# Kernel optimization log

Measured on AMD Instinct MI355X. Metric: run time of the kernel, lower is better.

Reference implementation:

```python
import jax, jax.numpy as jnp
import numpy as np

K = 5
NUM_CLASSES = 100


def setup_inputs() -> dict:
    key = jax.random.key(0)
    k1, k2, k3 = jax.random.split(key, 3)
    x = jax.random.normal(k1, (2048, 512), dtype=jnp.float32)
    x_train = jax.random.normal(k2, (65536, 512), dtype=jnp.float32)
    y_train = jax.random.randint(k3, (65536,), 0, NUM_CLASSES, dtype=jnp.int64)
    return {"x": x, "x_train": x_train, "y_train": y_train}


def reference(x, x_train, y_train):
    # Euclidean cdist via the expansion ||a-b||^2 = ||a||^2 + ||b||^2 - 2 a.b
    x2 = jnp.sum(x * x, axis=-1, keepdims=True)            # [B, 1]
    t2 = jnp.sum(x_train * x_train, axis=-1)               # [N]
    d2 = x2 + t2[None, :] - 2.0 * (x @ x_train.T)          # [B, N]
    dists = jnp.sqrt(jnp.maximum(d2, 0.0))
    # k smallest distances -> top_k of negated distances
    _, idx = jax.lax.top_k(-dists, K)                      # idx: [B, K]
    labels = y_train[idx]                                  # [B, K]
    # mode over the K neighbor labels via per-class vote counts;
    # argmax returns the smallest label among ties (matches torch.mode tie-break)
    counts = jnp.sum(jax.nn.one_hot(labels, NUM_CLASSES, dtype=jnp.int32), axis=1)  # [B, C]
    preds = jnp.argmax(counts, axis=-1)
    return preds
```

## Files before the change

kernel.cpp:

```cpp
#include <hip/hip_runtime.h>

#define NTRAIN 65536
#define NQ     2048
#define KD     512
#define KNN    5

#define QT2 256
#define TPB 2048
#define CH 256
#define NGRP (NTRAIN / TPB)
#define NQT2 (NQ / QT2)
#define NSLOT (NGRP * KNN)
#define MARGIN 2.0f
#define CAP 128

typedef short short8 __attribute__((ext_vector_type(8)));
typedef float f32x4 __attribute__((ext_vector_type(4)));

__device__ inline unsigned short f2bf(float f) {
    unsigned u = __float_as_uint(f);
    unsigned r = u + 0x7fffu + ((u >> 16) & 1u);
    return (unsigned short)(r >> 16);
}

template<int KK>
__device__ inline void ins5(float (&bd)[KK], int (&bi)[KK], float nd, int ni) {
    if (nd < bd[KK-1] || (nd == bd[KK-1] && ni < bi[KK-1])) {
#pragma unroll
        for (int k = 0; k < KK; ++k) {
            bool sw = (nd < bd[k]) || (nd == bd[k] && ni < bi[k]);
            float od = bd[k]; int oi = bi[k];
            bd[k] = sw ? nd : od; bi[k] = sw ? ni : oi;
            nd = sw ? od : nd;    ni = sw ? oi : ni;
        }
    }
}

__device__ inline void ins5v(float (&b5)[KNN], float v) {
    if (v < b5[KNN-1]) {
#pragma unroll
        for (int k = 0; k < KNN; ++k) {
            bool sw = v < b5[k];
            float o = b5[k];
            b5[k] = sw ? v : o;
            v = sw ? o : v;
        }
    }
}

__global__ __launch_bounds__(256)
void t2_kernel(const float* __restrict__ xt, float* __restrict__ t2) {
    int row  = blockIdx.x * 4 + (threadIdx.x >> 6);
    int lane = threadIdx.x & 63;
    const float4* p = (const float4*)(xt + (size_t)row * KD);
    float s = 0.f;
#pragma unroll
    for (int c = 0; c < 2; ++c) {
        float4 v = p[lane + c * 64];
        s += v.x * v.x + v.y * v.y + v.z * v.z + v.w * v.w;
    }
#pragma unroll
    for (int off = 32; off; off >>= 1) s += __shfl_down(s, off);
    if (lane == 0) t2[row] = s;
}

__global__ __launch_bounds__(256)
void conv_perm_kernel(const float* __restrict__ in, unsigned short* __restrict__ outp) {
    __shared__ unsigned short tile[16][512];
    const int rg = blockIdx.x, t = threadIdx.x;
    const int row_l = t >> 4, sub = t & 15;

    const float* rp = in + ((size_t)rg * 16 + row_l) * KD + sub * 4;
#pragma unroll
    for (int j = 0; j < 8; ++j) {
        float4 v = *(const float4*)(rp + j * 64);
        unsigned short us[4] = { f2bf(v.x), f2bf(v.y), f2bf(v.z), f2bf(v.w) };
        *(unsigned long long*)&tile[row_l][sub * 4 + j * 64] = *(const unsigned long long*)us;
    }
    __syncthreads();

    const int kt = t >> 4;
    unsigned short* ub = outp + (size_t)(((rg >> 4) * 16 + kt) * 16 + (rg & 15)) * 512;
#pragma unroll
    for (int i = 0; i < 4; ++i) {
        int l = sub * 4 + i;
        *(uint4*)(ub + l * 8) = *(const uint4*)&tile[l & 15][kt * 32 + ((l >> 4) << 3)];
    }
}

__global__ __launch_bounds__(1024)
void knn_filter(const unsigned short* __restrict__ xperm, const unsigned short* __restrict__ xtperm,
                const float* __restrict__ t2g,
                float* __restrict__ candD, int* __restrict__ candI) {
    __shared__ __align__(16) char smem[81920];

    const int tid  = threadIdx.x;
    const int w    = tid >> 6, lane = tid & 63;
    const int wm   = w & 3,  wn = w >> 2;
    const int lrow = lane & 15, lhi = lane >> 4;

    const int qt   = blockIdx.x >> 5;
    const int grp  = blockIdx.x & 31;
    const int q0   = qt * QT2;
    const int row0 = grp * TPB;

    const char* Au = (const char*)xtperm + (size_t)grp * (8 * 16 * 16 * 1024);
    const char* Bu = (const char*)xperm  + (size_t)qt  * (16 * 16 * 1024);
    const int laneOff = lane * 16;

    f32x4 acc[4][4];
#pragma unroll
    for (int m = 0; m < 4; ++m)
#pragma unroll
        for (int n = 0; n < 4; ++n) acc[m][n] = 0.f;

    float bd[4][KNN]; int bi[4][KNN];
#pragma unroll
    for (int n = 0; n < 4; ++n)
#pragma unroll
        for (int k = 0; k < KNN; ++k) { bd[n][k] = 3.4e38f; bi[n][k] = 0x7fffffff; }

    for (int ch = 0; ch < 8; ++ch) {
#pragma unroll 2
        for (int kt = 0; kt < 16; ++kt) {
            const char* Ak = Au + (size_t)(((ch * 16 + kt) * 16) + wm * 4) * 1024 + laneOff;
            const char* Bk = Bu + (size_t)((kt * 16) + wn * 4) * 1024 + laneOff;
            short8 a0 = *(const short8*)(Ak);
            short8 a1 = *(const short8*)(Ak + 1024);
            short8 a2 = *(const short8*)(Ak + 2048);
            short8 a3 = *(const short8*)(Ak + 3072);
            short8 b0 = *(const short8*)(Bk);
            short8 b1 = *(const short8*)(Bk + 1024);
            short8 b2 = *(const short8*)(Bk + 2048);
            short8 b3 = *(const short8*)(Bk + 3072);
            acc[0][0] = __builtin_amdgcn_mfma_f32_16x16x32_bf16(a0, b0, acc[0][0], 0, 0, 0);
            acc[0][1] = __builtin_amdgcn_mfma_f32_16x16x32_bf16(a0, b1, acc[0][1], 0, 0, 0);
            acc[0][2] = __builtin_amdgcn_mfma_f32_16x16x32_bf16(a0, b2, acc[0][2], 0, 0, 0);
            acc[0][3] = __builtin_amdgcn_mfma_f32_16x16x32_bf16(a0, b3, acc[0][3], 0, 0, 0);
            acc[1][0] = __builtin_amdgcn_mfma_f32_16x16x32_bf16(a1, b0, acc[1][0], 0, 0, 0);
            acc[1][1] = __builtin_amdgcn_mfma_f32_16x16x32_bf16(a1, b1, acc[1][1], 0, 0, 0);
            acc[1][2] = __builtin_amdgcn_mfma_f32_16x16x32_bf16(a1, b2, acc[1][2], 0, 0, 0);
            acc[1][3] = __builtin_amdgcn_mfma_f32_16x16x32_bf16(a1, b3, acc[1][3], 0, 0, 0);
            acc[2][0] = __builtin_amdgcn_mfma_f32_16x16x32_bf16(a2, b0, acc[2][0], 0, 0, 0);
            acc[2][1] = __builtin_amdgcn_mfma_f32_16x16x32_bf16(a2, b1, acc[2][1], 0, 0, 0);
            acc[2][2] = __builtin_amdgcn_mfma_f32_16x16x32_bf16(a2, b2, acc[2][2], 0, 0, 0);
            acc[2][3] = __builtin_amdgcn_mfma_f32_16x16x32_bf16(a2, b3, acc[2][3], 0, 0, 0);
            acc[3][0] = __builtin_amdgcn_mfma_f32_16x16x32_bf16(a3, b0, acc[3][0], 0, 0, 0);
            acc[3][1] = __builtin_amdgcn_mfma_f32_16x16x32_bf16(a3, b1, acc[3][1], 0, 0, 0);
            acc[3][2] = __builtin_amdgcn_mfma_f32_16x16x32_bf16(a3, b2, acc[3][2], 0, 0, 0);
            acc[3][3] = __builtin_amdgcn_mfma_f32_16x16x32_bf16(a3, b3, acc[3][3], 0, 0, 0);
        }

        {
            const int c0  = row0 + ch * CH;
            const int rbl = wm * 64 + lhi * 4;
#pragma unroll
            for (int m = 0; m < 4; ++m) {
                const float4 t2v = *(const float4*)(t2g + c0 + rbl + m * 16);
#pragma unroll
                for (int n = 0; n < 4; ++n)
#pragma unroll
                    for (int r2 = 0; r2 < 4; ++r2) {
                        float sc = fmaf(-2.f, acc[m][n][r2], (&t2v.x)[r2]);
                        ins5(bd[n], bi[n], sc, c0 + rbl + m * 16 + r2);
                    }
            }
#pragma unroll
            for (int m = 0; m < 4; ++m)
#pragma unroll
                for (int n = 0; n < 4; ++n) acc[m][n] = 0.f;
        }
    }

    float* MD = (float*)smem;
    int*   MI = (int*)(smem + 40960);
    const int slot = wm * 4 + lhi;
#pragma unroll
    for (int half = 0; half < 2; ++half) {
        __syncthreads();
#pragma unroll
        for (int n = 0; n < 4; ++n) {
            const int ql = wn * 64 + n * 16 + lrow;
            if ((ql >> 7) == half) {
#pragma unroll
                for (int k = 0; k < KNN; ++k) {
                    MD[(ql & 127) * 80 + slot * KNN + k] = bd[n][k];
                    MI[(ql & 127) * 80 + slot * KNN + k] = bi[n][k];
                }
            }
        }
        __syncthreads();
        if (tid < 128) {
            float fd[KNN]; int fi[KNN];
#pragma unroll
            for (int k = 0; k < KNN; ++k) { fd[k] = 3.4e38f; fi[k] = 0x7fffffff; }
            for (int j = 0; j < 16 * KNN; ++j) ins5(fd, fi, MD[tid * 80 + j], MI[tid * 80 + j]);
            size_t base = ((size_t)(q0 + half * 128 + tid) * NGRP + grp) * KNN;
#pragma unroll
            for (int k = 0; k < KNN; ++k) { candD[base + k] = fd[k]; candI[base + k] = fi[k]; }
        }
    }
}

__global__ __launch_bounds__(256)
void knn_refine(const float* __restrict__ x, const float* __restrict__ xt,
                const float* __restrict__ t2,
                const float* __restrict__ candD, const int* __restrict__ candI,
                const int* __restrict__ y, int* __restrict__ out) {
    __shared__ float sv[256 * KNN];
    __shared__ float sv2[64 * KNN];
    __shared__ float xl[KD];
    __shared__ int   lidx[CAP];
    __shared__ float lex[CAP];
    __shared__ int   lcount;
    __shared__ float sT;

    const int q = blockIdx.x, tid = threadIdx.x;
    const float* cd = candD + (size_t)q * NSLOT;
    const int*   ci = candI + (size_t)q * NSLOT;

    for (int i = tid; i < KD; i += 256) xl[i] = x[(size_t)q * KD + i];

    float b5[KNN];
#pragma unroll
    for (int k = 0; k < KNN; ++k) b5[k] = 3.4e38f;
    for (int j = tid; j < NSLOT; j += 256) ins5v(b5, cd[j]);
#pragma unroll
    for (int k = 0; k < KNN; ++k) sv[tid * KNN + k] = b5[k];
    __syncthreads();

    if (tid < 64) {
#pragma unroll
        for (int k = 0; k < KNN; ++k) b5[k] = 3.4e38f;
        for (int t = 0; t < 4; ++t)
#pragma unroll
            for (int k = 0; k < KNN; ++k) ins5v(b5, sv[(tid * 4 + t) * KNN + k]);
#pragma unroll
        for (int k = 0; k < KNN; ++k) sv2[tid * KNN + k] = b5[k];
    }
    __syncthreads();

    if (tid == 0) {
#pragma unroll
        for (int k = 0; k < KNN; ++k) b5[k] = 3.4e38f;
        for (int j = 0; j < 64 * KNN; ++j) ins5v(b5, sv2[j]);
        sT = b5[KNN - 1] + MARGIN;
        lcount = 0;
    }
    __syncthreads();
    float T = sT;

    for (int j = tid; j < NSLOT; j += 256) {
        if (cd[j] <= T) {
            int p = atomicAdd(&lcount, 1);
            if (p < CAP) lidx[p] = ci[j];
        }
    }
    __syncthreads();
    int Q = min(lcount, CAP);

    for (int j = tid; j < Q; j += 256) {
        int c = lidx[j];
        const float* tr = xt + (size_t)c * KD;
        float s = 0.f;
        for (int k = 0; k < KD; ++k) s = fmaf(xl[k], tr[k], s);
        lex[j] = fmaf(-2.f, s, t2[c]);
    }
    __syncthreads();

    if (tid == 0) {
        bool is64 = true;
#pragma unroll
        for (int i = 1; i < 64; i += 2) is64 = is64 && (y[i] == 0);
        float fd[KNN]; int fi[KNN];
#pragma unroll
        for (int k = 0; k < KNN; ++k) { fd[k] = 3.4e38f; fi[k] = 0x7fffffff; }
        for (int j = 0; j < Q; ++j) ins5(fd, fi, lex[j], lidx[j]);
        int lab[KNN];
#pragma unroll
        for (int k = 0; k < KNN; ++k) lab[k] = is64 ? y[2 * fi[k]] : y[fi[k]];
        int bestLab = 0x7fffffff, bestC = 0;
#pragma unroll
        for (int i = 0; i < KNN; ++i) {
            int c = 0;
#pragma unroll
            for (int j = 0; j < KNN; ++j) c += (lab[j] == lab[i]);
            if (c > bestC || (c == bestC && lab[i] < bestLab)) { bestC = c; bestLab = lab[i]; }
        }
        out[q] = bestLab;
    }
}

#define FB_QT 64
#define FB_TT 64
#define FB_KT 32
#define FB_NCHUNK 32
#define FB_CHUNK (NTRAIN / FB_NCHUNK)

__global__ __launch_bounds__(256)
void fb_knn_partial(const float* __restrict__ x, const float* __restrict__ xt,
                    const float* __restrict__ t2,
                    float* __restrict__ candD, int* __restrict__ candI) {
    __shared__ __align__(16) float smem[FB_QT * 81 * 2];
    float (*Xs)[FB_QT + 4] = (float (*)[FB_QT + 4])smem;
    float (*Ts)[FB_TT + 4] = (float (*)[FB_TT + 4])(smem + FB_KT * (FB_QT + 4));
    float (*MD)[81]     = (float (*)[81])smem;
    int   (*MI)[81]     = (int   (*)[81])(smem + FB_QT * 81);

    const int tid = threadIdx.x;
    const int tx = tid & 15, ty = tid >> 4;
    const int q0 = blockIdx.x * FB_QT;
    const int c0 = blockIdx.y * FB_CHUNK;
    const int sq = tid >> 2, sc = tid & 3;

    float bd[4][KNN]; int bi_[4][KNN];
#pragma unroll
    for (int i = 0; i < 4; ++i)
#pragma unroll
        for (int k = 0; k < KNN; ++k) { bd[i][k] = 3.4e38f; bi_[i][k] = 0x7fffffff; }

    const float* xrow = x + (size_t)(q0 + sq) * KD;

    for (int s = 0; s < FB_CHUNK; s += FB_TT) {
        float acc[4][4];
#pragma unroll
        for (int i = 0; i < 4; ++i)
#pragma unroll
            for (int j = 0; j < 4; ++j) acc[i][j] = 0.f;
        const float* trow = xt + (size_t)(c0 + s + sq) * KD;
        for (int kt = 0; kt < KD; kt += FB_KT) {
            float4 xv0 = *(const float4*)(xrow + kt + sc * 8);
            float4 xv1 = *(const float4*)(xrow + kt + sc * 8 + 4);
            float4 tv0 = *(const float4*)(trow + kt + sc * 8);
            float4 tv1 = *(const float4*)(trow + kt + sc * 8 + 4);
            __syncthreads();
            Xs[sc*8+0][sq] = xv0.x; Xs[sc*8+1][sq] = xv0.y;
            Xs[sc*8+2][sq] = xv0.z; Xs[sc*8+3][sq] = xv0.w;
            Xs[sc*8+4][sq] = xv1.x; Xs[sc*8+5][sq] = xv1.y;
            Xs[sc*8+6][sq] = xv1.z; Xs[sc*8+7][sq] = xv1.w;
            Ts[sc*8+0][sq] = tv0.x; Ts[sc*8+1][sq] = tv0.y;
            Ts[sc*8+2][sq] = tv0.z; Ts[sc*8+3][sq] = tv0.w;
            Ts[sc*8+4][sq] = tv1.x; Ts[sc*8+5][sq] = tv1.y;
            Ts[sc*8+6][sq] = tv1.z; Ts[sc*8+7][sq] = tv1.w;
            __syncthreads();
#pragma unroll
            for (int k = 0; k < FB_KT; ++k) {
                const float4 av = *(const float4*)&Xs[k][ty * 4];
                const float4 bv = *(const float4*)&Ts[k][tx * 4];
                float a[4] = {av.x, av.y, av.z, av.w};
                float b[4] = {bv.x, bv.y, bv.z, bv.w};
#pragma unroll
                for (int i = 0; i < 4; ++i)
#pragma unroll
                    for (int j = 0; j < 4; ++j)
                        acc[i][j] = fmaf(a[i], b[j], acc[i][j]);
            }
        }
#pragma unroll
        for (int j = 0; j < 4; ++j) {
            int tcol = c0 + s + tx * 4 + j;
            float tt = t2[tcol];
#pragma unroll
            for (int i = 0; i < 4; ++i)
                ins5(bd[i], bi_[i], fmaf(-2.0f, acc[i][j], tt), tcol);
        }
    }
    __syncthreads();
#pragma unroll
    for (int i = 0; i < 4; ++i)
#pragma unroll
        for (int k = 0; k < KNN; ++k) {
            MD[ty * 4 + i][tx * KNN + k] = bd[i][k];
            MI[ty * 4 + i][tx * KNN + k] = bi_[i][k];
        }
    __syncthreads();
    if (tid < FB_QT) {
        int q = q0 + tid;
        for (int k = 0; k < KNN; ++k) {
            float best = 3.4e38f; int bidx = 0x7fffffff; int bj = -1;
            for (int j = 0; j < 16 * KNN; ++j) {
                float dv = MD[tid][j]; int iv = MI[tid][j];
                if (dv < best || (dv == best && iv < bidx)) { best = dv; bidx = iv; bj = j; }
            }
            MD[tid][bj] = 3.4e38f;
            candD[((size_t)q * FB_NCHUNK + blockIdx.y) * KNN + k] = best;
            candI[((size_t)q * FB_NCHUNK + blockIdx.y) * KNN + k] = bidx;
        }
    }
}

__global__ __launch_bounds__(256)
void fb_knn_final(const float* __restrict__ candD, const int* __restrict__ candI,
                  const int* __restrict__ y, int* __restrict__ out) {
    int q = blockIdx.x * 256 + threadIdx.x;
    if (q >= NQ) return;
    bool is64 = true;
#pragma unroll
    for (int i = 1; i < 64; i += 2) is64 = is64 && (y[i] == 0);
    float bd[KNN]; int bi_[KNN];
#pragma unroll
    for (int k = 0; k < KNN; ++k) { bd[k] = 3.4e38f; bi_[k] = 0x7fffffff; }
    for (int c = 0; c < FB_NCHUNK * KNN; ++c)
        ins5(bd, bi_, candD[(size_t)q * FB_NCHUNK * KNN + c], candI[(size_t)q * FB_NCHUNK * KNN + c]);
    int lab[KNN];
#pragma unroll
    for (int k = 0; k < KNN; ++k) lab[k] = is64 ? y[2 * bi_[k]] : y[bi_[k]];
    int bestLab = 0x7fffffff, bestC = 0;
#pragma unroll
    for (int i = 0; i < KNN; ++i) {
        int c = 0;
#pragma unroll
        for (int j = 0; j < KNN; ++j) c += (lab[j] == lab[i]);
        if (c > bestC || (c == bestC && lab[i] < bestLab)) { bestC = c; bestLab = lab[i]; }
    }
    out[q] = bestLab;
}

extern "C" void kernel_launch(void* const* d_in, const int* in_sizes, int n_in,
                              void* d_out, int out_size, void* d_ws, size_t ws_size,
                              hipStream_t stream) {
    const float* x  = (const float*)d_in[0];
    const float* xt = (const float*)d_in[1];
    const int*   y  = (const int*)d_in[2];
    int* out = (int*)d_out;

    const size_t REQ = 72089600ull;
    if (ws_size >= REQ) {
        char* ws = (char*)d_ws;
        unsigned short* xt_pm = (unsigned short*)ws;
        unsigned short* x_pm  = (unsigned short*)(ws + 67108864);
        float*          t2    = (float*)(ws + 69206016);
        float*          candD = (float*)(ws + 69468160);
        int*            candI = (int*)(ws + 70778880);

        hipLaunchKernelGGL(conv_perm_kernel, dim3(NTRAIN / 16), dim3(256), 0, stream, xt, xt_pm);
        hipLaunchKernelGGL(conv_perm_kernel, dim3(NQ / 16), dim3(256), 0, stream, x, x_pm);
        hipLaunchKernelGGL(t2_kernel, dim3(NTRAIN / 4), dim3(256), 0, stream, xt, t2);
        hipLaunchKernelGGL(knn_filter, dim3(NQT2 * NGRP), dim3(1024), 0, stream,
                           x_pm, xt_pm, t2, candD, candI);
        hipLaunchKernelGGL(knn_refine, dim3(NQ), dim3(256), 0, stream,
                           x, xt, t2, candD, candI, y, out);
    } else {
        float* ws    = (float*)d_ws;
        float* t2    = ws;
        float* candD = ws + NTRAIN;
        int*   candI = (int*)(ws + NTRAIN + (size_t)NQ * FB_NCHUNK * KNN);
        hipLaunchKernelGGL(t2_kernel, dim3(NTRAIN / 4), dim3(256), 0, stream, xt, t2);
        hipLaunchKernelGGL(fb_knn_partial, dim3(NQ / FB_QT, FB_NCHUNK), dim3(256), 0, stream,
                           x, xt, t2, candD, candI);
        hipLaunchKernelGGL(fb_knn_final, dim3(NQ / 256), dim3(256), 0, stream,
                           candD, candI, y, out);
    }
}
```

Before: 527.2 us.

## Stage train tiles through double-buffered LDS and swap block index mapping

The train-side A operand is now loaded cooperatively into a double-buffered shared-memory tile, with a register prefetch two steps ahead. The four wm-waves that previously each loaded the same A fragments from global memory now read them from LDS. The block-to-(query tile, train group) mapping is swapped so that consecutive blocks share a train group, which is meant to improve L2 reuse of x_train. The cost is a __syncthreads every k-step, plus LDS traffic that competes with MFMA issue.

```diff
diff --git a/kernel.cpp b/kernel.cpp
--- a/kernel.cpp
+++ b/kernel.cpp
@@ -11,6 +11,7 @@
 #define NGRP (NTRAIN / TPB)
 #define NQT2 (NQ / QT2)
 #define NSLOT (NGRP * KNN)
+#define NSTEPS 128
 #define MARGIN 2.0f
 #define CAP 128
 
@@ -99,15 +100,18 @@
     const int wm   = w & 3,  wn = w >> 2;
     const int lrow = lane & 15, lhi = lane >> 4;
 
-    const int qt   = blockIdx.x >> 5;
-    const int grp  = blockIdx.x & 31;
+    const int qt   = blockIdx.x & 7;
+    const int grp  = blockIdx.x >> 3;
     const int q0   = qt * QT2;
     const int row0 = grp * TPB;
 
-    const char* Au = (const char*)xtperm + (size_t)grp * (8 * 16 * 16 * 1024);
-    const char* Bu = (const char*)xperm  + (size_t)qt  * (16 * 16 * 1024);
+    const char* Au = (const char*)xtperm + (size_t)grp * 2097152;
+    const char* Bu = (const char*)xperm  + (size_t)qt  * 262144;
     const int laneOff = lane * 16;
 
+    char* const Ab0 = smem;
+    char* const Ab1 = smem + 16384;
+
     f32x4 acc[4][4];
 #pragma unroll
     for (int m = 0; m < 4; ++m)
@@ -120,39 +124,50 @@
 #pragma unroll
         for (int k = 0; k < KNN; ++k) { bd[n][k] = 3.4e38f; bi[n][k] = 0x7fffffff; }
 
-    for (int ch = 0; ch < 8; ++ch) {
-#pragma unroll 2
-        for (int kt = 0; kt < 16; ++kt) {
-            const char* Ak = Au + (size_t)(((ch * 16 + kt) * 16) + wm * 4) * 1024 + laneOff;
-            const char* Bk = Bu + (size_t)((kt * 16) + wn * 4) * 1024 + laneOff;
-            short8 a0 = *(const short8*)(Ak);
-            short8 a1 = *(const short8*)(Ak + 1024);
-            short8 a2 = *(const short8*)(Ak + 2048);
-            short8 a3 = *(const short8*)(Ak + 3072);
-            short8 b0 = *(const short8*)(Bk);
-            short8 b1 = *(const short8*)(Bk + 1024);
-            short8 b2 = *(const short8*)(Bk + 2048);
-            short8 b3 = *(const short8*)(Bk + 3072);
-            acc[0][0] = __builtin_amdgcn_mfma_f32_16x16x32_bf16(a0, b0, acc[0][0], 0, 0, 0);
-            acc[0][1] = __builtin_amdgcn_mfma_f32_16x16x32_bf16(a0, b1, acc[0][1], 0, 0, 0);
-            acc[0][2] = __builtin_amdgcn_mfma_f32_16x16x32_bf16(a0, b2, acc[0][2], 0, 0, 0);
-            acc[0][3] = __builtin_amdgcn_mfma_f32_16x16x32_bf16(a0, b3, acc[0][3], 0, 0, 0);
-            acc[1][0] = __builtin_amdgcn_mfma_f32_16x16x32_bf16(a1, b0, acc[1][0], 0, 0, 0);
-            acc[1][1] = __builtin_amdgcn_mfma_f32_16x16x32_bf16(a1, b1, acc[1][1], 0, 0, 0);
-            acc[1][2] = __builtin_amdgcn_mfma_f32_16x16x32_bf16(a1, b2, acc[1][2], 0, 0, 0);
-            acc[1][3] = __builtin_amdgcn_mfma_f32_16x16x32_bf16(a1, b3, acc[1][3], 0, 0, 0);
-            acc[2][0] = __builtin_amdgcn_mfma_f32_16x16x32_bf16(a2, b0, acc[2][0], 0, 0, 0);
-            acc[2][1] = __builtin_amdgcn_mfma_f32_16x16x32_bf16(a2, b1, acc[2][1], 0, 0, 0);
-            acc[2][2] = __builtin_amdgcn_mfma_f32_16x16x32_bf16(a2, b2, acc[2][2], 0, 0, 0);
-            acc[2][3] = __builtin_amdgcn_mfma_f32_16x16x32_bf16(a2, b3, acc[2][3], 0, 0, 0);
-            acc[3][0] = __builtin_amdgcn_mfma_f32_16x16x32_bf16(a3, b0, acc[3][0], 0, 0, 0);
-            acc[3][1] = __builtin_amdgcn_mfma_f32_16x16x32_bf16(a3, b1, acc[3][1], 0, 0, 0);
-            acc[3][2] = __builtin_amdgcn_mfma_f32_16x16x32_bf16(a3, b2, acc[3][2], 0, 0, 0);
-            acc[3][3] = __builtin_amdgcn_mfma_f32_16x16x32_bf16(a3, b3, acc[3][3], 0, 0, 0);
-        }
-
-        {
-            const int c0  = row0 + ch * CH;
+    uint4 rgA = *(const uint4*)(Au + (size_t)(0 * 16 + w) * 1024 + laneOff);
+    *(uint4*)(Ab0 + w * 1024 + laneOff) = rgA;
+    rgA = *(const uint4*)(Au + (size_t)(1 * 16 + w) * 1024 + laneOff);
+    __syncthreads();
+
+    for (int s = 0; s < NSTEPS; ++s) {
+        char* const bufR = (s & 1) ? Ab1 : Ab0;
+        char* const bufW = (s & 1) ? Ab0 : Ab1;
+
+        if (s + 1 < NSTEPS) *(uint4*)(bufW + w * 1024 + laneOff) = rgA;
+        if (s + 2 < NSTEPS)
+            rgA = *(const uint4*)(Au + (size_t)((s + 2) * 16 + w) * 1024 + laneOff);
+
+        const int kt = s & 15;
+        const char* Bk = Bu + (size_t)((kt * 16) + wn * 4) * 1024 + laneOff;
+        short8 b0 = *(const short8*)(Bk);
+        short8 b1 = *(const short8*)(Bk + 1024);
+        short8 b2 = *(const short8*)(Bk + 2048);
+        short8 b3 = *(const short8*)(Bk + 3072);
+
+        short8 a0 = *(const short8*)(bufR + (wm * 4 + 0) * 1024 + laneOff);
+        short8 a1 = *(const short8*)(bufR + (wm * 4 + 1) * 1024 + laneOff);
+        short8 a2 = *(const short8*)(bufR + (wm * 4 + 2) * 1024 + laneOff);
+        short8 a3 = *(const short8*)(bufR + (wm * 4 + 3) * 1024 + laneOff);
+
+        acc[0][0] = __builtin_amdgcn_mfma_f32_16x16x32_bf16(a0, b0, acc[0][0], 0, 0, 0);
+        acc[0][1] = __builtin_amdgcn_mfma_f32_16x16x32_bf16(a0, b1, acc[0][1], 0, 0, 0);
+        acc[0][2] = __builtin_amdgcn_mfma_f32_16x16x32_bf16(a0, b2, acc[0][2], 0, 0, 0);
+        acc[0][3] = __builtin_amdgcn_mfma_f32_16x16x32_bf16(a0, b3, acc[0][3], 0, 0, 0);
+        acc[1][0] = __builtin_amdgcn_mfma_f32_16x16x32_bf16(a1, b0, acc[1][0], 0, 0, 0);
+        acc[1][1] = __builtin_amdgcn_mfma_f32_16x16x32_bf16(a1, b1, acc[1][1], 0, 0, 0);
+        acc[1][2] = __builtin_amdgcn_mfma_f32_16x16x32_bf16(a1, b2, acc[1][2], 0, 0, 0);
+        acc[1][3] = __builtin_amdgcn_mfma_f32_16x16x32_bf16(a1, b3, acc[1][3], 0, 0, 0);
+        acc[2][0] = __builtin_amdgcn_mfma_f32_16x16x32_bf16(a2, b0, acc[2][0], 0, 0, 0);
+        acc[2][1] = __builtin_amdgcn_mfma_f32_16x16x32_bf16(a2, b1, acc[2][1], 0, 0, 0);
+        acc[2][2] = __builtin_amdgcn_mfma_f32_16x16x32_bf16(a2, b2, acc[2][2], 0, 0, 0);
+        acc[2][3] = __builtin_amdgcn_mfma_f32_16x16x32_bf16(a2, b3, acc[2][3], 0, 0, 0);
+        acc[3][0] = __builtin_amdgcn_mfma_f32_16x16x32_bf16(a3, b0, acc[3][0], 0, 0, 0);
+        acc[3][1] = __builtin_amdgcn_mfma_f32_16x16x32_bf16(a3, b1, acc[3][1], 0, 0, 0);
+        acc[3][2] = __builtin_amdgcn_mfma_f32_16x16x32_bf16(a3, b2, acc[3][2], 0, 0, 0);
+        acc[3][3] = __builtin_amdgcn_mfma_f32_16x16x32_bf16(a3, b3, acc[3][3], 0, 0, 0);
+
+        if ((s & 15) == 15) {
+            const int c0  = row0 + (s >> 4) * CH;
             const int rbl = wm * 64 + lhi * 4;
 #pragma unroll
             for (int m = 0; m < 4; ++m) {
@@ -170,6 +185,8 @@
 #pragma unroll
                 for (int n = 0; n < 4; ++n) acc[m][n] = 0.f;
         }
+
+        __syncthreads();
     }
 
     float* MD = (float*)smem;
```

After: 756.2 us. +43.4%, slower.

## Switch filter GEMM from bf16 to fp8 MFMA with wider refine margin

Applied to the files above, without the earlier changes.

Converts the train and query matrices to fp8 instead of bf16 in the permute kernel and runs the candidate-filter GEMM with fp8 MFMA instructions. This halves the operand bytes streamed through the filter and uses the faster fp8 matrix path. To absorb the larger quantization error, the filter margin grows from 2 to 36 and the candidate cap from 128 to 192, so the exact fp32 refine stage does more work. If the margin does not cover fp8 error for some query, a true neighbour could be dropped.

```diff
diff --git a/kernel.cpp b/kernel.cpp
--- a/kernel.cpp
+++ b/kernel.cpp
@@ -11,11 +11,11 @@
 #define NGRP (NTRAIN / TPB)
 #define NQT2 (NQ / QT2)
 #define NSLOT (NGRP * KNN)
-#define MARGIN 2.0f
-#define CAP 128
-
-typedef short short8 __attribute__((ext_vector_type(8)));
+#define MARGIN 36.0f
+#define CAP 192
+
 typedef float f32x4 __attribute__((ext_vector_type(4)));
+typedef long lx2 __attribute__((ext_vector_type(2)));
 
 __device__ inline unsigned short f2bf(float f) {
     unsigned u = __float_as_uint(f);
@@ -65,8 +65,8 @@
 }
 
 __global__ __launch_bounds__(256)
-void conv_perm_kernel(const float* __restrict__ in, unsigned short* __restrict__ outp) {
-    __shared__ unsigned short tile[16][512];
+void conv_perm_fp8(const float* __restrict__ in, unsigned char* __restrict__ outp) {
+    __shared__ float tile[16][512];
     const int rg = blockIdx.x, t = threadIdx.x;
     const int row_l = t >> 4, sub = t & 15;
 
@@ -74,22 +74,30 @@
 #pragma unroll
     for (int j = 0; j < 8; ++j) {
         float4 v = *(const float4*)(rp + j * 64);
-        unsigned short us[4] = { f2bf(v.x), f2bf(v.y), f2bf(v.z), f2bf(v.w) };
-        *(unsigned long long*)&tile[row_l][sub * 4 + j * 64] = *(const unsigned long long*)us;
-    }
-    __syncthreads();
-
-    const int kt = t >> 4;
-    unsigned short* ub = outp + (size_t)(((rg >> 4) * 16 + kt) * 16 + (rg & 15)) * 512;
+        *(float4*)&tile[row_l][sub * 4 + j * 64] = v;
+    }
+    __syncthreads();
+
 #pragma unroll
     for (int i = 0; i < 4; ++i) {
-        int l = sub * 4 + i;
-        *(uint4*)(ub + l * 8) = *(const uint4*)&tile[l & 15][kt * 32 + ((l >> 4) << 3)];
+        const int sl = t + i * 256;
+        const int kt = sl >> 6, l = sl & 63;
+        const int row = l & 15;
+        const int kb  = kt * 32 + ((l >> 4) << 3);
+        const float* f = &tile[row][kb];
+        unsigned int w0 = 0, w1 = 0;
+        w0 = __builtin_amdgcn_cvt_pk_fp8_f32(f[0], f[1], w0, false);
+        w0 = __builtin_amdgcn_cvt_pk_fp8_f32(f[2], f[3], w0, true);
+        w1 = __builtin_amdgcn_cvt_pk_fp8_f32(f[4], f[5], w1, false);
+        w1 = __builtin_amdgcn_cvt_pk_fp8_f32(f[6], f[7], w1, true);
+        const int U = ((rg >> 4) * 16 + kt) * 16 + (rg & 15);
+        unsigned int* dst = (unsigned int*)(outp + (size_t)(U >> 1) * 1024 + l * 16 + (U & 1) * 8);
+        dst[0] = w0; dst[1] = w1;
     }
 }
 
 __global__ __launch_bounds__(1024)
-void knn_filter(const unsigned short* __restrict__ xperm, const unsigned short* __restrict__ xtperm,
+void knn_filter(const unsigned char* __restrict__ xperm, const unsigned char* __restrict__ xtperm,
                 const float* __restrict__ t2g,
                 float* __restrict__ candD, int* __restrict__ candI) {
     __shared__ __align__(16) char smem[81920];
@@ -104,8 +112,8 @@
     const int q0   = qt * QT2;
     const int row0 = grp * TPB;
 
-    const char* Au = (const char*)xtperm + (size_t)grp * (8 * 16 * 16 * 1024);
-    const char* Bu = (const char*)xperm  + (size_t)qt  * (16 * 16 * 1024);
+    const char* Au = (const char*)xtperm + (size_t)grp * 1048576;
+    const char* Bu = (const char*)xperm  + (size_t)qt  * 131072;
     const int laneOff = lane * 16;
 
     f32x4 acc[4][4];
@@ -123,32 +131,31 @@
     for (int ch = 0; ch < 8; ++ch) {
 #pragma unroll 2
         for (int kt = 0; kt < 16; ++kt) {
-            const char* Ak = Au + (size_t)(((ch * 16 + kt) * 16) + wm * 4) * 1024 + laneOff;
-            const char* Bk = Bu + (size_t)((kt * 16) + wn * 4) * 1024 + laneOff;
-            short8 a0 = *(const short8*)(Ak);
-            short8 a1 = *(const short8*)(Ak + 1024);
-            short8 a2 = *(const short8*)(Ak + 2048);
-            short8 a3 = *(const short8*)(Ak + 3072);
-            short8 b0 = *(const short8*)(Bk);
-            short8 b1 = *(const short8*)(Bk + 1024);
-            short8 b2 = *(const short8*)(Bk + 2048);
-            short8 b3 = *(const short8*)(Bk + 3072);
-            acc[0][0] = __builtin_amdgcn_mfma_f32_16x16x32_bf16(a0, b0, acc[0][0], 0, 0, 0);
-            acc[0][1] = __builtin_amdgcn_mfma_f32_16x16x32_bf16(a0, b1, acc[0][1], 0, 0, 0);
-            acc[0][2] = __builtin_amdgcn_mfma_f32_16x16x32_bf16(a0, b2, acc[0][2], 0, 0, 0);
-            acc[0][3] = __builtin_amdgcn_mfma_f32_16x16x32_bf16(a0, b3, acc[0][3], 0, 0, 0);
-            acc[1][0] = __builtin_amdgcn_mfma_f32_16x16x32_bf16(a1, b0, acc[1][0], 0, 0, 0);
-            acc[1][1] = __builtin_amdgcn_mfma_f32_16x16x32_bf16(a1, b1, acc[1][1], 0, 0, 0);
-            acc[1][2] = __builtin_amdgcn_mfma_f32_16x16x32_bf16(a1, b2, acc[1][2], 0, 0, 0);
-            acc[1][3] = __builtin_amdgcn_mfma_f32_16x16x32_bf16(a1, b3, acc[1][3], 0, 0, 0);
-            acc[2][0] = __builtin_amdgcn_mfma_f32_16x16x32_bf16(a2, b0, acc[2][0], 0, 0, 0);
-            acc[2][1] = __builtin_amdgcn_mfma_f32_16x16x32_bf16(a2, b1, acc[2][1], 0, 0, 0);
-            acc[2][2] = __builtin_amdgcn_mfma_f32_16x16x32_bf16(a2, b2, acc[2][2], 0, 0, 0);
-            acc[2][3] = __builtin_amdgcn_mfma_f32_16x16x32_bf16(a2, b3, acc[2][3], 0, 0, 0);
-            acc[3][0] = __builtin_amdgcn_mfma_f32_16x16x32_bf16(a3, b0, acc[3][0], 0, 0, 0);
-            acc[3][1] = __builtin_amdgcn_mfma_f32_16x16x32_bf16(a3, b1, acc[3][1], 0, 0, 0);
-            acc[3][2] = __builtin_amdgcn_mfma_f32_16x16x32_bf16(a3, b2, acc[3][2], 0, 0, 0);
-            acc[3][3] = __builtin_amdgcn_mfma_f32_16x16x32_bf16(a3, b3, acc[3][3], 0, 0, 0);
+            const int s = ch * 16 + kt;
+            const char* Ak = Au + (size_t)(s * 8 + wm * 2) * 1024 + laneOff;
+            const char* Bk = Bu + (size_t)(kt * 8 + wn * 2) * 1024 + laneOff;
+            lx2 A0 = *(const lx2*)(Ak);
+            lx2 A1 = *(const lx2*)(Ak + 1024);
+            lx2 B0 = *(const lx2*)(Bk);
+            lx2 B1 = *(const lx2*)(Bk + 1024);
+            long a0 = A0.x, a1 = A0.y, a2 = A1.x, a3 = A1.y;
+            long b0 = B0.x, b1 = B0.y, b2 = B1.x, b3 = B1.y;
+            acc[0][0] = __builtin_amdgcn_mfma_f32_16x16x32_fp8_fp8(a0, b0, acc[0][0], 0, 0, 0);
+            acc[0][1] = __builtin_amdgcn_mfma_f32_16x16x32_fp8_fp8(a0, b1, acc[0][1], 0, 0, 0);
+            acc[0][2] = __builtin_amdgcn_mfma_f32_16x16x32_fp8_fp8(a0, b2, acc[0][2], 0, 0, 0);
+            acc[0][3] = __builtin_amdgcn_mfma_f32_16x16x32_fp8_fp8(a0, b3, acc[0][3], 0, 0, 0);
+            acc[1][0] = __builtin_amdgcn_mfma_f32_16x16x32_fp8_fp8(a1, b0, acc[1][0], 0, 0, 0);
+            acc[1][1] = __builtin_amdgcn_mfma_f32_16x16x32_fp8_fp8(a1, b1, acc[1][1], 0, 0, 0);
+            acc[1][2] = __builtin_amdgcn_mfma_f32_16x16x32_fp8_fp8(a1, b2, acc[1][2], 0, 0, 0);
+            acc[1][3] = __builtin_amdgcn_mfma_f32_16x16x32_fp8_fp8(a1, b3, acc[1][3], 0, 0, 0);
+            acc[2][0] = __builtin_amdgcn_mfma_f32_16x16x32_fp8_fp8(a2, b0, acc[2][0], 0, 0, 0);
+            acc[2][1] = __builtin_amdgcn_mfma_f32_16x16x32_fp8_fp8(a2, b1, acc[2][1], 0, 0, 0);
+            acc[2][2] = __builtin_amdgcn_mfma_f32_16x16x32_fp8_fp8(a2, b2, acc[2][2], 0, 0, 0);
+            acc[2][3] = __builtin_amdgcn_mfma_f32_16x16x32_fp8_fp8(a2, b3, acc[2][3], 0, 0, 0);
+            acc[3][0] = __builtin_amdgcn_mfma_f32_16x16x32_fp8_fp8(a3, b0, acc[3][0], 0, 0, 0);
+            acc[3][1] = __builtin_amdgcn_mfma_f32_16x16x32_fp8_fp8(a3, b1, acc[3][1], 0, 0, 0);
+            acc[3][2] = __builtin_amdgcn_mfma_f32_16x16x32_fp8_fp8(a3, b2, acc[3][2], 0, 0, 0);
+            acc[3][3] = __builtin_amdgcn_mfma_f32_16x16x32_fp8_fp8(a3, b3, acc[3][3], 0, 0, 0);
         }
 
         {
@@ -424,20 +431,20 @@
     const int*   y  = (const int*)d_in[2];
     int* out = (int*)d_out;
 
-    const size_t REQ = 72089600ull;
+    const size_t REQ = 37486592ull;
     if (ws_size >= REQ) {
         char* ws = (char*)d_ws;
-        unsigned short* xt_pm = (unsigned short*)ws;
-        unsigned short* x_pm  = (unsigned short*)(ws + 67108864);
-        float*          t2    = (float*)(ws + 69206016);
-        float*          candD = (float*)(ws + 69468160);
-        int*            candI = (int*)(ws + 70778880);
-
-        hipLaunchKernelGGL(conv_perm_kernel, dim3(NTRAIN / 16), dim3(256), 0, stream, xt, xt_pm);
-        hipLaunchKernelGGL(conv_perm_kernel, dim3(NQ / 16), dim3(256), 0, stream, x, x_pm);
+        unsigned char* xt8 = (unsigned char*)ws;
+        unsigned char* x8  = (unsigned char*)(ws + 33554432);
+        float*         t2    = (float*)(ws + 34603008);
+        float*         candD = (float*)(ws + 34865152);
+        int*           candI = (int*)(ws + 36175872);
+
+        hipLaunchKernelGGL(conv_perm_fp8, dim3(NTRAIN / 16), dim3(256), 0, stream, xt, xt8);
+        hipLaunchKernelGGL(conv_perm_fp8, dim3(NQ / 16), dim3(256), 0, stream, x, x8);
         hipLaunchKernelGGL(t2_kernel, dim3(NTRAIN / 4), dim3(256), 0, stream, xt, t2);
         hipLaunchKernelGGL(knn_filter, dim3(NQT2 * NGRP), dim3(1024), 0, stream,
-                           x_pm, xt_pm, t2, candD, candI);
+                           x8, xt8, t2, candD, candI);
         hipLaunchKernelGGL(knn_refine, dim3(NQ), dim3(256), 0, stream,
                            x, xt, t2, candD, candI, y, out);
     } else {
```

Measured after the change: 440.5 us (median of 3 runs). 1.2x faster.
